# Optimization experiments

Measured on AMD Instinct MI355X. Metric: run time of the kernel, lower is better.

## Reference

```python
import jax, jax.numpy as jnp
import numpy as np

N_NODES = 100000
N_EDGES = 300000
N_GRAPHS = 4096
EMB = 256
L = 5
EPS = 1e-5


def setup_inputs() -> dict:
    key = jax.random.key(0)
    ks = jax.random.split(key, 16)
    x = jax.random.normal(ks[0], (N_NODES, 40), dtype=jnp.float32)
    edge_index = jax.random.randint(ks[1], (2, N_EDGES), 0, N_NODES, dtype=jnp.int32)
    edge_attr = jax.random.normal(ks[2], (N_EDGES, 10), dtype=jnp.float32)
    batch = jnp.sort(jax.random.randint(ks[3], (N_NODES,), 0, N_GRAPHS, dtype=jnp.int32))
    s = lambda fan: 1.0 / np.sqrt(fan)
    params = {
        "x_emb_W": jax.random.normal(ks[4], (EMB, 40), jnp.float32) * np.sqrt(2.0 / 40),
        "x_emb_b": jnp.zeros((EMB,), jnp.float32),
        "e_emb_W": jax.random.normal(ks[5], (EMB, 10), jnp.float32) * np.sqrt(2.0 / 10),
        "e_emb_b": jnp.zeros((EMB,), jnp.float32),
        "gcn_W": jax.random.normal(ks[6], (L, EMB, EMB), jnp.float32) * s(EMB),
        "gcn_b": jax.random.normal(ks[7], (L, EMB), jnp.float32) * s(EMB),
        "root_emb": jax.random.normal(ks[8], (L, EMB), jnp.float32),
        "bn_gamma": jnp.ones((L, EMB), jnp.float32),
        "bn_beta": jnp.zeros((L, EMB), jnp.float32),
        "p1_W": jax.random.normal(ks[9], (EMB // 2, EMB), jnp.float32) * s(EMB),
        "p1_b": jnp.zeros((EMB // 2,), jnp.float32),
        "p2_W": jax.random.normal(ks[10], (EMB // 2, EMB // 2), jnp.float32) * s(EMB // 2),
        "p2_b": jnp.zeros((EMB // 2,), jnp.float32),
        "p3_W": jax.random.normal(ks[11], (1, EMB // 2), jnp.float32) * s(EMB // 2),
        "p3_b": jnp.zeros((1,), jnp.float32),
    }
    return dict(x=x, edge_index=edge_index, edge_attr=edge_attr, batch=batch, **params)


def _gcn_conv(h, row, col, ea, W, b, root):
    # h: [N, D] node feats; ea: [E, D] edge feats
    hx = h @ W.T + b
    deg = jax.ops.segment_sum(jnp.ones_like(row, dtype=hx.dtype), row, num_segments=N_NODES) + 1.0
    dinv = deg ** -0.5
    norm = dinv[row] * dinv[col]                      # [E]
    msg = norm[:, None] * jax.nn.relu(hx[row] + ea)   # gather + relu + scale
    agg = jax.ops.segment_sum(msg, col, num_segments=N_NODES)  # scatter-add to targets
    return agg + jax.nn.relu(hx + root) / deg[:, None]


def _batchnorm(h, gamma, beta):
    mean = jnp.mean(h, axis=0)
    var = jnp.var(h, axis=0)
    return (h - mean) * jax.lax.rsqrt(var + EPS) * gamma + beta


def reference(x, edge_index, edge_attr, batch,
              x_emb_W, x_emb_b, e_emb_W, e_emb_b,
              gcn_W, gcn_b, root_emb, bn_gamma, bn_beta,
              p1_W, p1_b, p2_W, p2_b, p3_W, p3_b):
    row, col = edge_index[0], edge_index[1]
    h = x @ x_emb_W.T + x_emb_b
    ea = edge_attr @ e_emb_W.T + e_emb_b
    for l in range(L):
        h_in = h
        h = _gcn_conv(h, row, col, ea, gcn_W[l], gcn_b[l], root_emb[l])
        h = _batchnorm(h_in + h, bn_gamma[l], bn_beta[l])
        if l != L - 1:
            h = jax.nn.relu(h)
        # dropout is identity in eval mode
    # global mean pool over graphs
    sums = jax.ops.segment_sum(h, batch, num_segments=N_GRAPHS)
    cnts = jax.ops.segment_sum(jnp.ones((h.shape[0],), h.dtype), batch, num_segments=N_GRAPHS)
    g = sums / jnp.maximum(cnts, 1.0)[:, None]
    # prediction head: Lin-ReLU-Lin-ReLU-Lin
    g = jax.nn.relu(g @ p1_W.T + p1_b)
    g = jax.nn.relu(g @ p2_W.T + p2_b)
    return g @ p3_W.T + p3_b
```

## Files before the change

kernel.cpp:

```cpp
#include <hip/hip_runtime.h>
#include <hip/hip_bf16.h>

#define NN 100000
#define NE 300000
#define NG 4096
#define EMB 256
#define NLAYERS 5

typedef unsigned short u16;
typedef unsigned int u32;
typedef unsigned long long u64;

typedef short bf16x8 __attribute__((ext_vector_type(8)));
typedef float f32x4 __attribute__((ext_vector_type(4)));

__device__ __forceinline__ float b2f(u16 u){
    union { float f; u32 i; } v; v.i = ((u32)u) << 16; return v.f;
}
__device__ __forceinline__ u16 f2b(float f){
    __hip_bfloat16 h = __float2bfloat16(f);
    union { __hip_bfloat16 h; u16 u; } v; v.h = h; return v.u;
}

#define XNB 32
__global__ __launch_bounds__(256) void embed_x(const float* __restrict__ x,
        const float* __restrict__ W, const float* __restrict__ b,
        u16* __restrict__ t)
{
    __shared__ float sW[256][41];
    __shared__ float sx[XNB][40];
    int tid = threadIdx.x;
    for (int i = tid; i < 256*40; i += 256) sW[i/40][i%40] = W[i];
    int n0 = blockIdx.x * XNB;
    for (int i = tid; i < XNB*40; i += 256) {
        int j = i/40, k = i%40;
        sx[j][k] = x[(size_t)(n0+j)*40 + k];
    }
    __syncthreads();
    float bb = b[tid];
    for (int j = 0; j < XNB; ++j) {
        float a = bb;
        #pragma unroll
        for (int k = 0; k < 40; ++k) a = fmaf(sW[tid][k], sx[j][k], a);
        t[(size_t)(n0+j)*EMB + tid] = f2b(a);
    }
}

__global__ void wconv(const float* __restrict__ W, u16* __restrict__ Wb, int n)
{
    int i = blockIdx.x*256 + threadIdx.x;
    if (i < n) Wb[i] = f2b(W[i]);
}

__global__ void ewt_kernel(const float* __restrict__ eW, float* __restrict__ eWt)
{
    int i = blockIdx.x*256 + threadIdx.x;
    if (i < 2560) { int f = i/10, k = i%10; eWt[k*256 + f] = eW[i]; }
}

__global__ void hist_kernel(const int* __restrict__ row, const int* __restrict__ col,
        int* __restrict__ rcnt, int* __restrict__ ccnt, int E)
{
    int e = blockIdx.x*256 + threadIdx.x;
    if (e < E) {
        atomicAdd(&rcnt[row[e]], 1);
        atomicAdd(&ccnt[col[e]], 1);
    }
}

__global__ void deg_fin(const int* __restrict__ rcnt, float* __restrict__ dinv,
                        float* __restrict__ invdg, int N)
{
    int n = blockIdx.x*256 + threadIdx.x;
    if (n < N) {
        float d = (float)rcnt[n] + 1.0f;
        dinv[n]  = rsqrtf(d);
        invdg[n] = 1.0f/d;
    }
}

__global__ void scan1(const int* __restrict__ cnt, int* __restrict__ bsum, int N)
{
    __shared__ int sh[256];
    int t = threadIdx.x, i = blockIdx.x*256 + t;
    sh[t] = (i < N) ? cnt[i] : 0;
    __syncthreads();
    for (int off = 128; off > 0; off >>= 1) {
        if (t < off) sh[t] += sh[t+off];
        __syncthreads();
    }
    if (t == 0) bsum[blockIdx.x] = sh[0];
}

__global__ __launch_bounds__(512) void scan2(const int* __restrict__ bsum,
        int* __restrict__ bbase, int* __restrict__ coff, int nb)
{
    __shared__ int a[512], b[512];
    int t = threadIdx.x;
    a[t] = (t < nb) ? bsum[t] : 0;
    __syncthreads();
    int* src = a; int* dst = b;
    for (int off = 1; off < 512; off <<= 1) {
        dst[t] = (t >= off) ? src[t-off] + src[t] : src[t];
        __syncthreads();
        int* tmp = src; src = dst; dst = tmp;
    }
    bbase[t] = t ? src[t-1] : 0;
    if (t == 0) coff[NN] = NE;
}

__global__ void scan3(const int* __restrict__ cnt, const int* __restrict__ bbase,
        int* __restrict__ coff, int N)
{
    __shared__ int a[256], b[256];
    int t = threadIdx.x, i = blockIdx.x*256 + t;
    a[t] = (i < N) ? cnt[i] : 0;
    __syncthreads();
    int* src = a; int* dst = b;
    for (int off = 1; off < 256; off <<= 1) {
        dst[t] = (t >= off) ? src[t-off] + src[t] : src[t];
        __syncthreads();
        int* tmp = src; src = dst; dst = tmp;
    }
    if (i < N) coff[i] = bbase[blockIdx.x] + (t ? src[t-1] : 0);
}

__global__ void csr_fill(const int* __restrict__ row, const int* __restrict__ col,
        const float* __restrict__ eattr, const int* __restrict__ coff,
        const float* __restrict__ dinv, int* __restrict__ fill,
        int2* __restrict__ epack, u16* __restrict__ eab, int E)
{
    int e = blockIdx.x*256 + threadIdx.x;
    if (e < E) {
        int c = col[e], r = row[e];
        int p = coff[c] + atomicAdd(&fill[c], 1);
        int2 ep; ep.x = r; ep.y = __float_as_int(dinv[r] * dinv[c]);
        epack[p] = ep;
        #pragma unroll
        for (int k = 0; k < 10; ++k) eab[(size_t)p*16 + k] = f2b(eattr[(size_t)e*10 + k]);
        #pragma unroll
        for (int k = 10; k < 16; ++k) eab[(size_t)p*16 + k] = 0;
    }
}

#define CS_STRIDE 144
__global__ __launch_bounds__(512) void gemm_mfma(const u16* __restrict__ A,
        const u16* __restrict__ Wb, const float* __restrict__ bias,
        const float* __restrict__ bnsc, int doBN,
        u16* __restrict__ C, int M)
{
    __shared__ __align__(16) char smem[51200];
    u16* As = (u16*)smem;
    u16* Bs = (u16*)(smem + 16384);
    float* scS = (float*)(smem + 49152);
    float* shS = scS + 256;
    const int tid = threadIdx.x;
    if (doBN && tid < 256) { scS[tid] = bnsc[tid]; shS[tid] = bnsc[256+tid]; }
    const int wid  = tid >> 6;
    const int lane = tid & 63;
    const int wm = wid >> 2, wn = wid & 3;
    const int m0 = blockIdx.x * 128;
    const int r8 = tid >> 3;
    const int ch = tid & 7;
    const int sw = ch ^ (r8 & 7);
    const int ga0 = min(m0 + r8,      M-1);
    const int ga1 = min(m0 + r8 + 64, M-1);

    uint4 ra[2], rb[4];
    #define LOADK(k0) do {                                                     \
        ra[0] = *reinterpret_cast<const uint4*>(&A[(size_t)ga0*256 + (k0) + ch*8]); \
        ra[1] = *reinterpret_cast<const uint4*>(&A[(size_t)ga1*256 + (k0) + ch*8]); \
        rb[0] = *reinterpret_cast<const uint4*>(&Wb[(size_t)(r8+  0)*256 + (k0) + ch*8]); \
        rb[1] = *reinterpret_cast<const uint4*>(&Wb[(size_t)(r8+ 64)*256 + (k0) + ch*8]); \
        rb[2] = *reinterpret_cast<const uint4*>(&Wb[(size_t)(r8+128)*256 + (k0) + ch*8]); \
        rb[3] = *reinterpret_cast<const uint4*>(&Wb[(size_t)(r8+192)*256 + (k0) + ch*8]); \
    } while(0)

    LOADK(0);
    if (doBN) __syncthreads();
    f32x4 acc[4][4] = {};
    for (int k0 = 0; k0 < 256; k0 += 64) {
        uint4 va0 = ra[0], va1 = ra[1];
        if (doBN) {
            int kk = k0 + ch*8;
            u32 w0[4] = {va0.x, va0.y, va0.z, va0.w};
            u32 w1[4] = {va1.x, va1.y, va1.z, va1.w};
            #pragma unroll
            for (int j = 0; j < 4; ++j) {
                float l0 = b2f((u16)(w0[j] & 0xffffu)), h0 = b2f((u16)(w0[j] >> 16));
                float l1 = b2f((u16)(w1[j] & 0xffffu)), h1 = b2f((u16)(w1[j] >> 16));
                float s0 = scS[kk+2*j], s1 = scS[kk+2*j+1];
                float b0 = shS[kk+2*j], b1 = shS[kk+2*j+1];
                l0 = fmaxf(fmaf(l0, s0, b0), 0.f); h0 = fmaxf(fmaf(h0, s1, b1), 0.f);
                l1 = fmaxf(fmaf(l1, s0, b0), 0.f); h1 = fmaxf(fmaf(h1, s1, b1), 0.f);
                w0[j] = (u32)f2b(l0) | ((u32)f2b(h0) << 16);
                w1[j] = (u32)f2b(l1) | ((u32)f2b(h1) << 16);
            }
            va0.x=w0[0]; va0.y=w0[1]; va0.z=w0[2]; va0.w=w0[3];
            va1.x=w1[0]; va1.y=w1[1]; va1.z=w1[2]; va1.w=w1[3];
        }
        *reinterpret_cast<uint4*>(&As[((r8     )*8 + sw)*8]) = va0;
        *reinterpret_cast<uint4*>(&As[((r8 + 64)*8 + sw)*8]) = va1;
        *reinterpret_cast<uint4*>(&Bs[((r8     )*8 + sw)*8]) = rb[0];
        *reinterpret_cast<uint4*>(&Bs[((r8+ 64 )*8 + sw)*8]) = rb[1];
        *reinterpret_cast<uint4*>(&Bs[((r8+128 )*8 + sw)*8]) = rb[2];
        *reinterpret_cast<uint4*>(&Bs[((r8+192 )*8 + sw)*8]) = rb[3];
        __syncthreads();
        if (k0 < 192) LOADK(k0 + 64);
        const int c = lane >> 4;
        const int rl = lane & 15;
        #pragma unroll
        for (int kt = 0; kt < 2; ++kt) {
            bf16x8 af[4], bfr[4];
            #pragma unroll
            for (int f = 0; f < 4; ++f) {
                int rA = wm*64 + f*16 + rl;
                int cha = (kt*4 + c) ^ (rA & 7);
                af[f] = *reinterpret_cast<const bf16x8*>(&As[(rA*8 + cha)*8]);
                int rB = wn*64 + f*16 + rl;
                int chb = (kt*4 + c) ^ (rB & 7);
                bfr[f] = *reinterpret_cast<const bf16x8*>(&Bs[(rB*8 + chb)*8]);
            }
            #pragma unroll
            for (int fm = 0; fm < 4; ++fm)
                #pragma unroll
                for (int fn = 0; fn < 4; ++fn)
                    acc[fm][fn] = __builtin_amdgcn_mfma_f32_16x16x32_bf16(
                        af[fm], bfr[fn], acc[fm][fn], 0, 0, 0);
        }
        __syncthreads();
    }
    #undef LOADK

    u16* Cs = (u16*)smem;
    const int cn = lane & 15, rq = lane >> 4;
    #pragma unroll
    for (int pp = 0; pp < 2; ++pp) {
        if ((wn >> 1) == pp) {
            int cl0 = (wn & 1)*64;
            #pragma unroll
            for (int fn = 0; fn < 4; ++fn) {
                int n = wn*64 + fn*16 + cn;
                float bb = bias[n];
                #pragma unroll
                for (int fm = 0; fm < 4; ++fm) {
                    int rbase = wm*64 + fm*16 + rq*4;
                    #pragma unroll
                    for (int r = 0; r < 4; ++r)
                        Cs[(rbase + r)*CS_STRIDE + cl0 + fn*16 + cn] =
                            f2b(acc[fm][fn][r] + bb);
                }
            }
        }
        __syncthreads();
        #pragma unroll
        for (int it = 0; it < 4; ++it) {
            int idx = tid + it*512;
            int rowi = idx >> 4;
            int c8  = (idx & 15) * 8;
            int m = m0 + rowi;
            if (m < M)
                *reinterpret_cast<uint4*>(&C[(size_t)m*256 + pp*128 + c8]) =
                    *reinterpret_cast<const uint4*>(&Cs[rowi*CS_STRIDE + c8]);
        }
        __syncthreads();
    }
}

#define GFB 4
#define NGROUPS (NN/GFB)
__global__ __launch_bounds__(256) void gather_combine_w(const int2* __restrict__ epack,
        const u16* __restrict__ eab, const int* __restrict__ coff,
        const float* __restrict__ eWt, const float* __restrict__ ebv,
        const u16* __restrict__ hx, const float* __restrict__ rootv,
        const float* __restrict__ invdg, const float* __restrict__ bnscPrev,
        int doBN, u16* __restrict__ t, float* __restrict__ stats, int N)
{
    __shared__ float red[4][512];
    const int wid = threadIdx.x >> 6, lane = threadIdx.x & 63;
    const int f4 = lane*4;
    float w[4][10], bb[4];
    #pragma unroll
    for (int k = 0; k < 10; ++k) {
        float4 wv = *reinterpret_cast<const float4*>(&eWt[k*256 + f4]);
        w[0][k] = wv.x; w[1][k] = wv.y; w[2][k] = wv.z; w[3][k] = wv.w;
    }
    { float4 bv = *reinterpret_cast<const float4*>(&ebv[f4]);
      bb[0]=bv.x; bb[1]=bv.y; bb[2]=bv.z; bb[3]=bv.w; }
    float4 root = *reinterpret_cast<const float4*>(&rootv[f4]);
    float sc[4] = {1,1,1,1}, sh[4] = {0,0,0,0};
    if (doBN) {
        float4 s = *reinterpret_cast<const float4*>(&bnscPrev[f4]);
        float4 b = *reinterpret_cast<const float4*>(&bnscPrev[256+f4]);
        sc[0]=s.x; sc[1]=s.y; sc[2]=s.z; sc[3]=s.w;
        sh[0]=b.x; sh[1]=b.y; sh[2]=b.z; sh[3]=b.w;
    }
    float sacc[4] = {0,0,0,0}, s2acc[4] = {0,0,0,0};

    for (int g = blockIdx.x*4 + wid; g < NGROUPS; g += gridDim.x*4) {
        const int nb = g*GFB;
        int c1 = coff[nb+1], c2 = coff[nb+2], c3 = coff[nb+3], c4 = coff[nb+4];
        int s = coff[nb], e = c4;
        int jn = 0, cend = c1;
        float acc[4] = {0,0,0,0};

        #define FLUSH() do {                                                   \
            int n_ = nb + jn;                                                  \
            size_t idx_ = (size_t)n_*EMB + f4;                                 \
            uint2 hv_ = *reinterpret_cast<const uint2*>(&t[idx_]);             \
            uint2 xv_ = *reinterpret_cast<const uint2*>(&hx[idx_]);            \
            float id_ = invdg[n_];                                             \
            float hh_[4] = { b2f((u16)(hv_.x&0xffffu)), b2f((u16)(hv_.x>>16)), \
                             b2f((u16)(hv_.y&0xffffu)), b2f((u16)(hv_.y>>16)) };\
            float xx_[4] = { b2f((u16)(xv_.x&0xffffu)), b2f((u16)(xv_.x>>16)), \
                             b2f((u16)(xv_.y&0xffffu)), b2f((u16)(xv_.y>>16)) };\
            float rt_[4] = { root.x, root.y, root.z, root.w };                 \
            u16 ov_[4];                                                        \
            _Pragma("unroll")                                                  \
            for (int jj = 0; jj < 4; ++jj) {                                   \
                float hin_ = hh_[jj];                                          \
                if (doBN) hin_ = fmaxf(fmaf(hin_, sc[jj], sh[jj]), 0.f);       \
                float rv_ = xx_[jj] + rt_[jj];                                 \
                rv_ = rv_ > 0.f ? rv_ : 0.f;                                   \
                float tv_ = hin_ + acc[jj] + rv_*id_;                          \
                ov_[jj] = f2b(tv_);                                            \
                sacc[jj] += tv_; s2acc[jj] += tv_*tv_;                         \
                acc[jj] = 0.f;                                                 \
            }                                                                  \
            uint2 o_; o_.x = (u32)ov_[0] | ((u32)ov_[1]<<16);                  \
            o_.y = (u32)ov_[2] | ((u32)ov_[3]<<16);                            \
            *reinterpret_cast<uint2*>(&t[idx_]) = o_;                          \
            ++jn; cend = (jn==1) ? c2 : (jn==2) ? c3 : c4;                     \
        } while(0)

        #define CONSUME(nm, hvv, alo, ahi) do {                                \
            float hf_[4] = { b2f((u16)((hvv).x&0xffffu)), b2f((u16)((hvv).x>>16)),\
                             b2f((u16)((hvv).y&0xffffu)), b2f((u16)((hvv).y>>16)) };\
            float at_[10];                                                     \
            at_[0]=b2f((u16)((alo).x&0xffffu)); at_[1]=b2f((u16)((alo).x>>16));\
            at_[2]=b2f((u16)((alo).y&0xffffu)); at_[3]=b2f((u16)((alo).y>>16));\
            at_[4]=b2f((u16)((alo).z&0xffffu)); at_[5]=b2f((u16)((alo).z>>16));\
            at_[6]=b2f((u16)((alo).w&0xffffu)); at_[7]=b2f((u16)((alo).w>>16));\
            at_[8]=b2f((u16)((ahi).x&0xffffu)); at_[9]=b2f((u16)((ahi).x>>16));\
            _Pragma("unroll")                                                  \
            for (int jj = 0; jj < 4; ++jj) {                                   \
                float ea_ = bb[jj];                                            \
                _Pragma("unroll")                                              \
                for (int k = 0; k < 10; ++k) ea_ = fmaf(at_[k], w[jj][k], ea_);\
                float v_ = hf_[jj] + ea_;                                      \
                acc[jj] += v_ > 0.f ? v_*(nm) : 0.f;                           \
            }                                                                  \
        } while(0)

        int p = s;
        for (; p + 4 <= e; p += 4) {
            int2 e0 = epack[p], e1 = epack[p+1], e2 = epack[p+2], e3 = epack[p+3];
            uint2 h0 = *reinterpret_cast<const uint2*>(&hx[(size_t)e0.x*EMB + f4]);
            uint2 h1 = *reinterpret_cast<const uint2*>(&hx[(size_t)e1.x*EMB + f4]);
            uint2 h2 = *reinterpret_cast<const uint2*>(&hx[(size_t)e2.x*EMB + f4]);
            uint2 h3 = *reinterpret_cast<const uint2*>(&hx[(size_t)e3.x*EMB + f4]);
            uint4 a0l = *reinterpret_cast<const uint4*>(&eab[(size_t)(p+0)*16]);
            uint4 a0h = *reinterpret_cast<const uint4*>(&eab[(size_t)(p+0)*16+8]);
            uint4 a1l = *reinterpret_cast<const uint4*>(&eab[(size_t)(p+1)*16]);
            uint4 a1h = *reinterpret_cast<const uint4*>(&eab[(size_t)(p+1)*16+8]);
            uint4 a2l = *reinterpret_cast<const uint4*>(&eab[(size_t)(p+2)*16]);
            uint4 a2h = *reinterpret_cast<const uint4*>(&eab[(size_t)(p+2)*16+8]);
            uint4 a3l = *reinterpret_cast<const uint4*>(&eab[(size_t)(p+3)*16]);
            uint4 a3h = *reinterpret_cast<const uint4*>(&eab[(size_t)(p+3)*16+8]);
            while (p+0 >= cend) FLUSH();
            CONSUME(__int_as_float(e0.y), h0, a0l, a0h);
            while (p+1 >= cend) FLUSH();
            CONSUME(__int_as_float(e1.y), h1, a1l, a1h);
            while (p+2 >= cend) FLUSH();
            CONSUME(__int_as_float(e2.y), h2, a2l, a2h);
            while (p+3 >= cend) FLUSH();
            CONSUME(__int_as_float(e3.y), h3, a3l, a3h);
        }
        for (; p < e; ++p) {
            int2 e0 = epack[p];
            uint2 h0 = *reinterpret_cast<const uint2*>(&hx[(size_t)e0.x*EMB + f4]);
            uint4 a0l = *reinterpret_cast<const uint4*>(&eab[(size_t)p*16]);
            uint4 a0h = *reinterpret_cast<const uint4*>(&eab[(size_t)p*16+8]);
            while (p >= cend) FLUSH();
            CONSUME(__int_as_float(e0.y), h0, a0l, a0h);
        }
        while (jn < GFB) FLUSH();
        #undef FLUSH
        #undef CONSUME
    }

    #pragma unroll
    for (int j = 0; j < 4; ++j) {
        red[wid][f4+j]     = sacc[j];
        red[wid][256+f4+j] = s2acc[j];
    }
    __syncthreads();
    int tt = threadIdx.x;
    float a0 = red[0][tt] + red[1][tt] + red[2][tt] + red[3][tt];
    float a1 = red[0][256+tt] + red[1][256+tt] + red[2][256+tt] + red[3][256+tt];
    atomicAdd(&stats[tt], a0);
    atomicAdd(&stats[256+tt], a1);
}

__global__ void bn_finalize(const float* __restrict__ stats,
        const float* __restrict__ gamma, const float* __restrict__ beta,
        float* __restrict__ sc, int N)
{
    int f = threadIdx.x;
    float inv = 1.0f / (float)N;
    float mean = stats[f] * inv;
    float var  = stats[256+f] * inv - mean*mean;
    float is = rsqrtf(var + 1e-5f);
    float scale = gamma[f] * is;
    sc[f] = scale;
    sc[256+f] = fmaf(-mean, scale, beta[f]);
}

__global__ __launch_bounds__(256) void pool_kernel(const u16* __restrict__ t,
        const int* __restrict__ batch, const float* __restrict__ bnsc4,
        float* __restrict__ psum, float* __restrict__ pcnt, int N)
{
    int tid = threadIdx.x;
    int half = tid >> 7;
    int pp = tid & 127;
    const u32* t32 = (const u32*)t;
    float sc0 = bnsc4[2*pp],     sc1 = bnsc4[2*pp+1];
    float sh0 = bnsc4[256+2*pp], sh1 = bnsc4[256+2*pp+1];
    int n0 = blockIdx.x * 256;
    int n1 = min(n0 + 256, N);
    int start = n0 + half;
    if (start >= n1) return;
    int cur = batch[start];
    float a0 = 0.f, a1 = 0.f;
    int cnt = 0;
    for (int n = start; n < n1; n += 2) {
        int gb = batch[n];
        if (gb != cur) {
            atomicAdd(&psum[(size_t)cur*EMB + 2*pp],   a0);
            atomicAdd(&psum[(size_t)cur*EMB + 2*pp+1], a1);
            if (pp == 0) atomicAdd(&pcnt[cur], (float)cnt);
            a0 = a1 = 0.f; cnt = 0; cur = gb;
        }
        u32 v = t32[(size_t)n*128 + pp];
        a0 += fmaf(b2f((u16)(v & 0xffffu)), sc0, sh0);
        a1 += fmaf(b2f((u16)(v >> 16)),     sc1, sh1);
        ++cnt;
    }
    atomicAdd(&psum[(size_t)cur*EMB + 2*pp],   a0);
    atomicAdd(&psum[(size_t)cur*EMB + 2*pp+1], a1);
    if (pp == 0) atomicAdd(&pcnt[cur], (float)cnt);
}

__global__ void pool2g(const float* __restrict__ psum, const float* __restrict__ pcnt,
        u16* __restrict__ gbf)
{
    int i = blockIdx.x*256 + threadIdx.x;
    if (i < NG*128) {
        int g = i >> 7, p2 = (i & 127)*2;
        float invc = 1.0f / fmaxf(pcnt[g], 1.0f);
        u32 pk = (u32)f2b(psum[(size_t)g*EMB + p2] * invc)
               | ((u32)f2b(psum[(size_t)g*EMB + p2 + 1] * invc) << 16);
        ((u32*)gbf)[i] = pk;
    }
}

__global__ __launch_bounds__(256) void gemm_head(const u16* __restrict__ A,
        const u16* __restrict__ W, const float* __restrict__ bias,
        u16* __restrict__ C, int M, int K)
{
    __shared__ u16 As[128*64];
    __shared__ u16 Bs[128*64];
    const int tid  = threadIdx.x;
    const int wid  = tid >> 6;
    const int lane = tid & 63;
    const int wr = wid >> 1, wc = wid & 1;
    const int m0 = blockIdx.x * 128;
    f32x4 acc[4][4] = {};
    for (int k0 = 0; k0 < K; k0 += 64) {
        #pragma unroll
        for (int i = 0; i < 4; ++i) {
            int L = tid + i*256;
            int rowi = L >> 3, ch = L & 7;
            int sw = ch ^ (rowi & 7);
            int gr = m0 + rowi; gr = gr < M ? gr : M-1;
            uint4 va = *reinterpret_cast<const uint4*>(&A[(size_t)gr*K + k0 + ch*8]);
            *reinterpret_cast<uint4*>(&As[(rowi*8 + sw)*8]) = va;
            uint4 vb = *reinterpret_cast<const uint4*>(&W[(size_t)rowi*K + k0 + ch*8]);
            *reinterpret_cast<uint4*>(&Bs[(rowi*8 + sw)*8]) = vb;
        }
        __syncthreads();
        const int c = lane >> 4;
        const int rl = lane & 15;
        #pragma unroll
        for (int kt = 0; kt < 2; ++kt) {
            bf16x8 af[4], bfr[4];
            #pragma unroll
            for (int f = 0; f < 4; ++f) {
                int ra = wr*64 + f*16 + rl;
                int cha = (kt*4 + c) ^ (ra & 7);
                af[f] = *reinterpret_cast<const bf16x8*>(&As[(ra*8 + cha)*8]);
                int rb = wc*64 + f*16 + rl;
                int chb = (kt*4 + c) ^ (rb & 7);
                bfr[f] = *reinterpret_cast<const bf16x8*>(&Bs[(rb*8 + chb)*8]);
            }
            #pragma unroll
            for (int fm = 0; fm < 4; ++fm)
                #pragma unroll
                for (int fn = 0; fn < 4; ++fn)
                    acc[fm][fn] = __builtin_amdgcn_mfma_f32_16x16x32_bf16(
                        af[fm], bfr[fn], acc[fm][fn], 0, 0, 0);
        }
        __syncthreads();
    }
    const int cn = lane & 15, rq = lane >> 4;
    #pragma unroll
    for (int fn = 0; fn < 4; ++fn) {
        int n = wc*64 + fn*16 + cn;
        float bb = bias[n];
        #pragma unroll
        for (int fm = 0; fm < 4; ++fm) {
            #pragma unroll
            for (int r = 0; r < 4; ++r) {
                int m = m0 + wr*64 + fm*16 + rq*4 + r;
                if (m < M) C[(size_t)m*128 + n] = f2b(fmaxf(acc[fm][fn][r] + bb, 0.f));
            }
        }
    }
}

__global__ __launch_bounds__(256) void head_final(const u16* __restrict__ h2,
        const float* __restrict__ p3W, const float* __restrict__ p3b,
        float* __restrict__ out, int G)
{
    int tid = blockIdx.x*256 + threadIdx.x;
    int g = tid >> 4, sub = tid & 15;
    if (g >= G) return;
    uint4 v = *reinterpret_cast<const uint4*>(&h2[(size_t)g*128 + sub*8]);
    u32 wv[4] = {v.x, v.y, v.z, v.w};
    float s = 0.f;
    #pragma unroll
    for (int j = 0; j < 4; ++j) {
        s = fmaf(b2f((u16)(wv[j] & 0xffffu)), p3W[sub*8 + 2*j],   s);
        s = fmaf(b2f((u16)(wv[j] >> 16)),     p3W[sub*8 + 2*j+1], s);
    }
    s += __shfl_down(s, 8, 16);
    s += __shfl_down(s, 4, 16);
    s += __shfl_down(s, 2, 16);
    s += __shfl_down(s, 1, 16);
    if (sub == 0) out[g] = s + p3b[0];
}

extern "C" void kernel_launch(void* const* d_in, const int* in_sizes, int n_in,
                              void* d_out, int out_size, void* d_ws, size_t ws_size,
                              hipStream_t stream)
{
    const float* x     = (const float*)d_in[0];
    const int*   eidx  = (const int*)d_in[1];
    const float* eattr = (const float*)d_in[2];
    const int*   batch = (const int*)d_in[3];
    const float* xW    = (const float*)d_in[4];
    const float* xb    = (const float*)d_in[5];
    const float* eW    = (const float*)d_in[6];
    const float* eb    = (const float*)d_in[7];
    const float* gcnW  = (const float*)d_in[8];
    const float* gcnb  = (const float*)d_in[9];
    const float* rootE = (const float*)d_in[10];
    const float* bng   = (const float*)d_in[11];
    const float* bnb   = (const float*)d_in[12];
    const float* p1W   = (const float*)d_in[13];
    const float* p1b   = (const float*)d_in[14];
    const float* p2W   = (const float*)d_in[15];
    const float* p2b   = (const float*)d_in[16];
    const float* p3W   = (const float*)d_in[17];
    const float* p3b   = (const float*)d_in[18];
    float* out = (float*)d_out;

    const int* row = eidx;
    const int* col = eidx + NE;

    const size_t HSZ = (size_t)NN * EMB;
    const int NWB = 5*EMB*EMB;

    char* p = (char*)d_ws;
    u16* t   = (u16*)p;            p += HSZ*2;
    u16* hx  = (u16*)p;            p += HSZ*2;
    u16* Wb  = (u16*)p;            p += (size_t)NWB*2;
    float* eWt = (float*)p;        p += 2560*4;
    char* zbase = p;
    int* rcnt   = (int*)p;         p += (size_t)NN*4;
    int* ccnt   = (int*)p;         p += (size_t)NN*4;
    int* fill   = (int*)p;         p += (size_t)NN*4;
    float* stats= (float*)p;       p += (size_t)NLAYERS*512*4;
    float* psum = (float*)p;       p += (size_t)NG*EMB*4;
    float* pcnt = (float*)p;       p += (size_t)NG*4;
    size_t zbytes = (size_t)(p - zbase);
    float* dinv = (float*)p;       p += (size_t)NN*4;
    float* invdg= (float*)p;       p += (size_t)NN*4;
    float* bnscA= (float*)p;       p += (size_t)NLAYERS*512*4;
    int* coff   = (int*)p;         p += (size_t)(NN+1)*4;
    int* bsum   = (int*)p;         p += 512*4;
    int* bbase  = (int*)p;         p += 512*4;
    int2* epack = (int2*)p;        p += (size_t)NE*8;
    u16* eab    = (u16*)p;         p += (size_t)NE*16*2;
    u16* gbf    = (u16*)p;         p += (size_t)NG*EMB*2;
    u16* h1b    = (u16*)p;         p += (size_t)NG*128*2;
    u16* h2b    = (u16*)p;         p += (size_t)NG*128*2;
    u16* Wh1    = (u16*)p;         p += (size_t)128*256*2;
    u16* Wh2    = (u16*)p;         p += (size_t)128*128*2;
    size_t NEED = (size_t)(p - (char*)d_ws);
    if (ws_size < NEED) return;

    hipMemsetAsync(zbase, 0, zbytes, stream);

    const int NBS = (NN + 255)/256;

    embed_x<<<NN/XNB, 256, 0, stream>>>(x, xW, xb, t);
    wconv<<<(NWB+255)/256, 256, 0, stream>>>(gcnW, Wb, NWB);
    wconv<<<(128*256+255)/256, 256, 0, stream>>>(p1W, Wh1, 128*256);
    wconv<<<(128*128+255)/256, 256, 0, stream>>>(p2W, Wh2, 128*128);
    ewt_kernel<<<10, 256, 0, stream>>>(eW, eWt);
    hist_kernel<<<(NE+255)/256, 256, 0, stream>>>(row, col, rcnt, ccnt, NE);
    deg_fin<<<NBS, 256, 0, stream>>>(rcnt, dinv, invdg, NN);
    scan1<<<NBS, 256, 0, stream>>>(ccnt, bsum, NN);
    scan2<<<1, 512, 0, stream>>>(bsum, bbase, coff, NBS);
    scan3<<<NBS, 256, 0, stream>>>(ccnt, bbase, coff, NN);
    csr_fill<<<(NE+255)/256, 256, 0, stream>>>(row, col, eattr, coff, dinv, fill,
                                               epack, eab, NE);

    for (int l = 0; l < NLAYERS; ++l) {
        const u16*   Wl = Wb + (size_t)l*EMB*EMB;
        const float* bl = gcnb + (size_t)l*EMB;
        const float* rl = rootE + (size_t)l*EMB;
        const float* scPrev = bnscA + (size_t)(l > 0 ? l-1 : 0)*512;
        int doBN = (l > 0) ? 1 : 0;
        gemm_mfma<<<(NN+127)/128, 512, 0, stream>>>(t, Wl, bl, scPrev, doBN, hx, NN);
        gather_combine_w<<<2048, 256, 0, stream>>>(epack, eab, coff, eWt, eb,
                hx, rl, invdg, scPrev, doBN, t, stats + l*512, NN);
        bn_finalize<<<1, 256, 0, stream>>>(stats + l*512, bng + (size_t)l*EMB,
                                           bnb + (size_t)l*EMB, bnscA + (size_t)l*512, NN);
    }

    pool_kernel<<<NBS, 256, 0, stream>>>(t, batch, bnscA + (size_t)(NLAYERS-1)*512,
                                         psum, pcnt, NN);
    pool2g<<<(NG*128+255)/256, 256, 0, stream>>>(psum, pcnt, gbf);
    gemm_head<<<NG/128, 256, 0, stream>>>(gbf, Wh1, p1b, h1b, NG, 256);
    gemm_head<<<NG/128, 256, 0, stream>>>(h1b, Wh2, p2b, h2b, NG, 128);
    head_final<<<(NG*16+255)/256, 256, 0, stream>>>(h2b, p3W, p3b, out, NG);
}
```

Before: 991.6 us.

## Fold BN finalize into consumers and read GEMM weights directly from global

Removes the separate single-block bn_finalize launch per layer by recomputing BN scale/shift from raw stats inside the GEMM, gather and pool kernels. The GEMM no longer stages the weight tile in shared memory; each wave loads B fragments straight from global (cache-resident) memory, cutting LDS use and per-tile stores and barriers. The gather grid is also reduced from 2048 to 1536 blocks. Trade-offs are redundant per-block BN math and uncoalesced global weight reads in the MFMA inner loop.

```diff
diff --git a/kernel.cpp b/kernel.cpp
--- a/kernel.cpp
+++ b/kernel.cpp
@@ -9,7 +9,6 @@
 
 typedef unsigned short u16;
 typedef unsigned int u32;
-typedef unsigned long long u64;
 
 typedef short bf16x8 __attribute__((ext_vector_type(8)));
 typedef float f32x4 __attribute__((ext_vector_type(4)));
@@ -20,6 +19,17 @@
 __device__ __forceinline__ u16 f2b(float f){
     __hip_bfloat16 h = __float2bfloat16(f);
     union { __hip_bfloat16 h; u16 u; } v; v.h = h; return v.u;
+}
+__device__ __forceinline__ void bnsc_f(const float* __restrict__ stats,
+        const float* __restrict__ gamma, const float* __restrict__ beta,
+        int f, float& sc, float& sh)
+{
+    const float inv = 1.0f / (float)NN;
+    float mean = stats[f] * inv;
+    float var  = stats[256+f] * inv - mean*mean;
+    float is = rsqrtf(var + 1e-5f);
+    sc = gamma[f] * is;
+    sh = fmaf(-mean, sc, beta[f]);
 }
 
 #define XNB 32
@@ -146,16 +156,19 @@
 #define CS_STRIDE 144
 __global__ __launch_bounds__(512) void gemm_mfma(const u16* __restrict__ A,
         const u16* __restrict__ Wb, const float* __restrict__ bias,
-        const float* __restrict__ bnsc, int doBN,
+        const float* __restrict__ stats, const float* __restrict__ gamma,
+        const float* __restrict__ beta, int doBN,
         u16* __restrict__ C, int M)
 {
-    __shared__ __align__(16) char smem[51200];
+    __shared__ __align__(16) char smem[38912];
     u16* As = (u16*)smem;
-    u16* Bs = (u16*)(smem + 16384);
-    float* scS = (float*)(smem + 49152);
+    float* scS = (float*)(smem + 36864);
     float* shS = scS + 256;
     const int tid = threadIdx.x;
-    if (doBN && tid < 256) { scS[tid] = bnsc[tid]; shS[tid] = bnsc[256+tid]; }
+    if (doBN && tid < 256) {
+        float s, h; bnsc_f(stats, gamma, beta, tid, s, h);
+        scS[tid] = s; shS[tid] = h;
+    }
     const int wid  = tid >> 6;
     const int lane = tid & 63;
     const int wm = wid >> 2, wn = wid & 3;
@@ -166,21 +179,20 @@
     const int ga0 = min(m0 + r8,      M-1);
     const int ga1 = min(m0 + r8 + 64, M-1);
 
-    uint4 ra[2], rb[4];
+    uint4 ra0, ra1;
     #define LOADK(k0) do {                                                     \
-        ra[0] = *reinterpret_cast<const uint4*>(&A[(size_t)ga0*256 + (k0) + ch*8]); \
-        ra[1] = *reinterpret_cast<const uint4*>(&A[(size_t)ga1*256 + (k0) + ch*8]); \
-        rb[0] = *reinterpret_cast<const uint4*>(&Wb[(size_t)(r8+  0)*256 + (k0) + ch*8]); \
-        rb[1] = *reinterpret_cast<const uint4*>(&Wb[(size_t)(r8+ 64)*256 + (k0) + ch*8]); \
-        rb[2] = *reinterpret_cast<const uint4*>(&Wb[(size_t)(r8+128)*256 + (k0) + ch*8]); \
-        rb[3] = *reinterpret_cast<const uint4*>(&Wb[(size_t)(r8+192)*256 + (k0) + ch*8]); \
+        ra0 = *reinterpret_cast<const uint4*>(&A[(size_t)ga0*256 + (k0) + ch*8]); \
+        ra1 = *reinterpret_cast<const uint4*>(&A[(size_t)ga1*256 + (k0) + ch*8]); \
     } while(0)
 
     LOADK(0);
     if (doBN) __syncthreads();
     f32x4 acc[4][4] = {};
+    const int c = lane >> 4;
+    const int rl = lane & 15;
+    const int nb0 = wn*64 + rl;
     for (int k0 = 0; k0 < 256; k0 += 64) {
-        uint4 va0 = ra[0], va1 = ra[1];
+        uint4 va0 = ra0, va1 = ra1;
         if (doBN) {
             int kk = k0 + ch*8;
             u32 w0[4] = {va0.x, va0.y, va0.z, va0.w};
@@ -201,25 +213,18 @@
         }
         *reinterpret_cast<uint4*>(&As[((r8     )*8 + sw)*8]) = va0;
         *reinterpret_cast<uint4*>(&As[((r8 + 64)*8 + sw)*8]) = va1;
-        *reinterpret_cast<uint4*>(&Bs[((r8     )*8 + sw)*8]) = rb[0];
-        *reinterpret_cast<uint4*>(&Bs[((r8+ 64 )*8 + sw)*8]) = rb[1];
-        *reinterpret_cast<uint4*>(&Bs[((r8+128 )*8 + sw)*8]) = rb[2];
-        *reinterpret_cast<uint4*>(&Bs[((r8+192 )*8 + sw)*8]) = rb[3];
         __syncthreads();
         if (k0 < 192) LOADK(k0 + 64);
-        const int c = lane >> 4;
-        const int rl = lane & 15;
         #pragma unroll
         for (int kt = 0; kt < 2; ++kt) {
             bf16x8 af[4], bfr[4];
             #pragma unroll
             for (int f = 0; f < 4; ++f) {
+                bfr[f] = *reinterpret_cast<const bf16x8*>(
+                    &Wb[(size_t)(nb0 + f*16)*256 + k0 + (kt*4 + c)*8]);
                 int rA = wm*64 + f*16 + rl;
                 int cha = (kt*4 + c) ^ (rA & 7);
                 af[f] = *reinterpret_cast<const bf16x8*>(&As[(rA*8 + cha)*8]);
-                int rB = wn*64 + f*16 + rl;
-                int chb = (kt*4 + c) ^ (rB & 7);
-                bfr[f] = *reinterpret_cast<const bf16x8*>(&Bs[(rB*8 + chb)*8]);
             }
             #pragma unroll
             for (int fm = 0; fm < 4; ++fm)
@@ -273,7 +278,8 @@
         const u16* __restrict__ eab, const int* __restrict__ coff,
         const float* __restrict__ eWt, const float* __restrict__ ebv,
         const u16* __restrict__ hx, const float* __restrict__ rootv,
-        const float* __restrict__ invdg, const float* __restrict__ bnscPrev,
+        const float* __restrict__ invdg, const float* __restrict__ statsPrev,
+        const float* __restrict__ gammaPrev, const float* __restrict__ betaPrev,
         int doBN, u16* __restrict__ t, float* __restrict__ stats, int N)
 {
     __shared__ float red[4][512];
@@ -290,10 +296,9 @@
     float4 root = *reinterpret_cast<const float4*>(&rootv[f4]);
     float sc[4] = {1,1,1,1}, sh[4] = {0,0,0,0};
     if (doBN) {
-        float4 s = *reinterpret_cast<const float4*>(&bnscPrev[f4]);
-        float4 b = *reinterpret_cast<const float4*>(&bnscPrev[256+f4]);
-        sc[0]=s.x; sc[1]=s.y; sc[2]=s.z; sc[3]=s.w;
-        sh[0]=b.x; sh[1]=b.y; sh[2]=b.z; sh[3]=b.w;
+        #pragma unroll
+        for (int j = 0; j < 4; ++j)
+            bnsc_f(statsPrev, gammaPrev, betaPrev, f4+j, sc[j], sh[j]);
     }
     float sacc[4] = {0,0,0,0}, s2acc[4] = {0,0,0,0};
 
@@ -402,30 +407,18 @@
     atomicAdd(&stats[256+tt], a1);
 }
 
-__global__ void bn_finalize(const float* __restrict__ stats,
-        const float* __restrict__ gamma, const float* __restrict__ beta,
-        float* __restrict__ sc, int N)
-{
-    int f = threadIdx.x;
-    float inv = 1.0f / (float)N;
-    float mean = stats[f] * inv;
-    float var  = stats[256+f] * inv - mean*mean;
-    float is = rsqrtf(var + 1e-5f);
-    float scale = gamma[f] * is;
-    sc[f] = scale;
-    sc[256+f] = fmaf(-mean, scale, beta[f]);
-}
-
 __global__ __launch_bounds__(256) void pool_kernel(const u16* __restrict__ t,
-        const int* __restrict__ batch, const float* __restrict__ bnsc4,
+        const int* __restrict__ batch, const float* __restrict__ stats5,
+        const float* __restrict__ gamma5, const float* __restrict__ beta5,
         float* __restrict__ psum, float* __restrict__ pcnt, int N)
 {
     int tid = threadIdx.x;
     int half = tid >> 7;
     int pp = tid & 127;
     const u32* t32 = (const u32*)t;
-    float sc0 = bnsc4[2*pp],     sc1 = bnsc4[2*pp+1];
-    float sh0 = bnsc4[256+2*pp], sh1 = bnsc4[256+2*pp+1];
+    float sc0, sh0, sc1, sh1;
+    bnsc_f(stats5, gamma5, beta5, 2*pp,   sc0, sh0);
+    bnsc_f(stats5, gamma5, beta5, 2*pp+1, sc1, sh1);
     int n0 = blockIdx.x * 256;
     int n1 = min(n0 + 256, N);
     int start = n0 + half;
@@ -596,7 +589,6 @@
     size_t zbytes = (size_t)(p - zbase);
     float* dinv = (float*)p;       p += (size_t)NN*4;
     float* invdg= (float*)p;       p += (size_t)NN*4;
-    float* bnscA= (float*)p;       p += (size_t)NLAYERS*512*4;
     int* coff   = (int*)p;         p += (size_t)(NN+1)*4;
     int* bsum   = (int*)p;         p += 512*4;
     int* bbase  = (int*)p;         p += 512*4;
@@ -631,17 +623,19 @@
         const u16*   Wl = Wb + (size_t)l*EMB*EMB;
         const float* bl = gcnb + (size_t)l*EMB;
         const float* rl = rootE + (size_t)l*EMB;
-        const float* scPrev = bnscA + (size_t)(l > 0 ? l-1 : 0)*512;
+        const float* stPrev = stats + (size_t)(l > 0 ? l-1 : 0)*512;
+        const float* gmPrev = bng + (size_t)(l > 0 ? l-1 : 0)*EMB;
+        const float* btPrev = bnb + (size_t)(l > 0 ? l-1 : 0)*EMB;
         int doBN = (l > 0) ? 1 : 0;
-        gemm_mfma<<<(NN+127)/128, 512, 0, stream>>>(t, Wl, bl, scPrev, doBN, hx, NN);
-        gather_combine_w<<<2048, 256, 0, stream>>>(epack, eab, coff, eWt, eb,
-                hx, rl, invdg, scPrev, doBN, t, stats + l*512, NN);
-        bn_finalize<<<1, 256, 0, stream>>>(stats + l*512, bng + (size_t)l*EMB,
-                                           bnb + (size_t)l*EMB, bnscA + (size_t)l*512, NN);
-    }
-
-    pool_kernel<<<NBS, 256, 0, stream>>>(t, batch, bnscA + (size_t)(NLAYERS-1)*512,
-                                         psum, pcnt, NN);
+        gemm_mfma<<<(NN+127)/128, 512, 0, stream>>>(t, Wl, bl, stPrev, gmPrev,
+                                                    btPrev, doBN, hx, NN);
+        gather_combine_w<<<1536, 256, 0, stream>>>(epack, eab, coff, eWt, eb,
+                hx, rl, invdg, stPrev, gmPrev, btPrev, doBN, t, stats + l*512, NN);
+    }
+
+    pool_kernel<<<NBS, 256, 0, stream>>>(t, batch, stats + (size_t)(NLAYERS-1)*512,
+            bng + (size_t)(NLAYERS-1)*EMB, bnb + (size_t)(NLAYERS-1)*EMB,
+            psum, pcnt, NN);
     pool2g<<<(NG*128+255)/256, 256, 0, stream>>>(psum, pcnt, gbf);
     gemm_head<<<NG/128, 256, 0, stream>>>(gbf, Wh1, p1b, h1b, NG, 256);
     gemm_head<<<NG/128, 256, 0, stream>>>(h1b, Wh2, p2b, h2b, NG, 128);
```

New measurement: 944.7 us. 1.05x faster.
